# Performance work log

Measured on AMD Instinct MI355X. Metric: run time of the kernel, lower is better.

Reference implementation:

```python
import jax, jax.numpy as jnp
import numpy as np

RES = 300          # grid resolution per axis
NC_D = 16          # density_n_comp
NC_A = 48          # app_n_comp
APP_DIM = 27       # app_dim
N = 500000         # number of ray samples

MAT_MODE = [[0, 1], [0, 2], [1, 2]]
VEC_MODE = [2, 1, 0]


def setup_inputs() -> dict:
    key = jax.random.key(0)
    k0, k1, k2, k3 = jax.random.split(key, 4)
    xyz_sampled = jax.random.uniform(k0, (N, 3), minval=-1.0, maxval=1.0, dtype=jnp.float32)
    plane_coef = 0.1 * jax.random.normal(k1, (3, NC_A + NC_D, RES, RES), dtype=jnp.float32)
    line_coef = 0.1 * jax.random.normal(k2, (3, NC_A + NC_D, RES, 1), dtype=jnp.float32)
    basis_W = jax.random.normal(k3, (APP_DIM, 3 * NC_A), dtype=jnp.float32) / np.sqrt(3 * NC_A)
    return {"xyz_sampled": xyz_sampled, "plane_coef": plane_coef,
            "line_coef": line_coef, "basis_W": basis_W}


def _grid_sample(img, x, y):
    """Bilinear grid_sample, align_corners=True, zeros padding.
    img: (C, H, W); x, y: (N,) normalized coords in [-1, 1] (x -> W, y -> H).
    Returns (C, N)."""
    C, H, W = img.shape
    ix = (x + 1.0) * 0.5 * (W - 1)
    iy = (y + 1.0) * 0.5 * (H - 1)
    x0f = jnp.floor(ix)
    y0f = jnp.floor(iy)
    wx = ix - x0f   # weight for x0+1
    wy = iy - y0f   # weight for y0+1
    x0 = x0f.astype(jnp.int32)
    y0 = y0f.astype(jnp.int32)
    out = jnp.zeros((C, x.shape[0]), img.dtype)
    for dx, wxc in ((0, 1.0 - wx), (1, wx)):
        for dy, wyc in ((0, 1.0 - wy), (1, wy)):
            xi = x0 + dx
            yi = y0 + dy
            valid = (xi >= 0) & (xi < W) & (yi >= 0) & (yi < H)
            xic = jnp.clip(xi, 0, W - 1)
            yic = jnp.clip(yi, 0, H - 1)
            w = jnp.where(valid, wxc * wyc, 0.0)
            out = out + img[:, yic, xic] * w
    return out


def reference(xyz_sampled, plane_coef, line_coef, basis_W):
    zeros = jnp.zeros((xyz_sampled.shape[0],), xyz_sampled.dtype)
    pf, lf = [], []
    for i in range(3):
        m0, m1 = MAT_MODE[i]
        # plane: grid = (x=xyz[m0] -> W, y=xyz[m1] -> H)
        pf.append(_grid_sample(plane_coef[i], xyz_sampled[:, m0], xyz_sampled[:, m1]))
        # line: grid = (x=0 -> W(=1), y=xyz[vecMode] -> H) => 1D interp along H
        lf.append(_grid_sample(line_coef[i], zeros, xyz_sampled[:, VEC_MODE[i]]))
    pf = jnp.stack(pf)  # (3, NC_A+NC_D, N)
    lf = jnp.stack(lf)  # (3, NC_A+NC_D, N)
    # compute_densityfeature: last density_n_comp channels, multiply and sum-reduce
    sigma_feature = jnp.sum(pf[:, NC_A:] * lf[:, NC_A:], axis=(0, 1))  # (N,)
    # compute_appfeature: first app_n_comp channels, multiply then basis projection
    app_feats = (pf[:, :NC_A] * lf[:, :NC_A]).reshape(3 * NC_A, -1)    # (3*NC_A, N)
    app_features = app_feats.T @ basis_W.T                              # (N, APP_DIM)
    return sigma_feature, app_features
```

## Files before the change

### kernel.cpp

```cpp
#include <hip/hip_runtime.h>
#include <hip/hip_bf16.h>

#define RES 300
#define NPLANE (RES * RES)
#define NC_A 48
#define APP_DIM 27
#define KDIM 144
#define KS 168

#define NPBLK 4219

__device__ __forceinline__ float bf_lo(unsigned int u) { return __uint_as_float(u << 16); }
__device__ __forceinline__ float bf_hi(unsigned int u) { return __uint_as_float(u & 0xffff0000u); }

__global__ __launch_bounds__(256) void prep(
    const float* __restrict__ plane, const float* __restrict__ line,
    const float* __restrict__ W,
    uint2* __restrict__ TpV, unsigned int* __restrict__ TlP,
    __hip_bfloat16* __restrict__ Wg) {
  __shared__ unsigned int ltile[64 * 65];
  const int blk = blockIdx.x;
  const int tid = threadIdx.x;

  if (blk < NPBLK) {
    int flat = blk * 256 + tid;
    if (flat < 1080000) {
      int c4   = flat & 15;
      int rest = flat >> 4;
      int i  = (rest >= 45000) ? 2 : (rest >= 22500 ? 1 : 0);
      int p0 = (rest - i * 22500) * 4;
      const float* src = plane + (size_t)(i * 64 + c4 * 4) * NPLANE + p0;
      float4 r0 = *(const float4*)(src);
      float4 r1 = *(const float4*)(src + NPLANE);
      float4 r2 = *(const float4*)(src + 2 * NPLANE);
      float4 r3 = *(const float4*)(src + 3 * NPLANE);
      const float* rr[4] = {&r0.x, &r1.x, &r2.x, &r3.x};
      #pragma unroll
      for (int k = 0; k < 4; ++k) {
        __hip_bfloat162 h0, h1;
        h0.x = __float2bfloat16(rr[0][k]);
        h0.y = __float2bfloat16(rr[1][k]);
        h1.x = __float2bfloat16(rr[2][k]);
        h1.y = __float2bfloat16(rr[3][k]);
        uint2 u;
        u.x = *(unsigned int*)&h0;
        u.y = *(unsigned int*)&h1;
        TpV[((size_t)i * NPLANE + p0 + k) * 16 + c4] = u;
      }
    }
  } else if (blk < NPBLK + 15) {
    const int b  = blk - NPBLK;
    const int i  = b / 5;
    const int y0 = (b % 5) * 64;
    const int yl = tid & 63;
    const int cq = tid >> 6;
    #pragma unroll
    for (int k = 0; k < 16; ++k) {
      int c = cq * 16 + k;
      int y = y0 + yl;
      float a = 0.f, bv = 0.f;
      if (y < RES) {
        const float* row = line + (i * 64 + c) * RES;
        a  = row[y];
        bv = row[min(y + 1, RES - 1)];
      }
      __hip_bfloat162 h;
      h.x = __float2bfloat16(a);
      h.y = __float2bfloat16(bv);
      ltile[yl * 65 + c] = *(unsigned int*)&h;
    }
    __syncthreads();
    #pragma unroll
    for (int k = 0; k < 16; ++k) {
      int ylc = k * 4 + cq;
      int c   = tid & 63;
      int y   = y0 + ylc;
      if (y < RES) TlP[((size_t)i * RES + y) * 64 + c] = ltile[ylc * 65 + c];
    }
  } else {
    for (int idx = tid; idx < 2 * 5 * 64 * 8; idx += 256) {
      int j    = idx & 7;
      int lane = (idx >> 3) & 63;
      int kt   = (idx >> 9) % 5;
      int tile = idx / (5 * 64 * 8);
      int n = tile * 16 + (lane & 15);
      int k = kt * 32 + (lane >> 4) * 8 + j;
      float v = (n < APP_DIM && k < KDIM) ? W[n * KDIM + k] : 0.f;
      Wg[idx] = __float2bfloat16(v);
    }
  }
}

typedef __attribute__((ext_vector_type(8))) short short8;
typedef __attribute__((ext_vector_type(4))) float f32x4;

__global__ __launch_bounds__(256, 6) void tensorf_main(
    const float* __restrict__ xyz, const unsigned int* __restrict__ TpU,
    const unsigned int* __restrict__ TlP, const __hip_bfloat16* __restrict__ Wg,
    float* __restrict__ out, int n_total) {
  __shared__ __hip_bfloat16 prod[64 * KS];
  __shared__ float cw[64 * 18];

  const int tid  = threadIdx.x;
  const int lane = tid & 63;
  const int wave = tid >> 6;
  const int n0   = blockIdx.x * 64;

  for (int j = tid; j < 64 * 12; j += 256) {
    int s = j / 12, kk = (j % 12) * 2;
    *(unsigned int*)&prod[s * KS + KDIM + kk] = 0u;
  }

  if (tid < 64) {
    int n = min(n0 + tid, n_total - 1);
    float crd[3] = {xyz[3 * n], xyz[3 * n + 1], xyz[3 * n + 2]};
    const int m0s[3] = {0, 0, 1}, m1s[3] = {1, 2, 2}, vms[3] = {2, 1, 0};
    float* c = &cw[tid * 18];
    #pragma unroll
    for (int i = 0; i < 3; ++i) {
      float ix = fminf(fmaxf((crd[m0s[i]] + 1.f) * 149.5f, 0.f), 299.f);
      float iy = fminf(fmaxf((crd[m1s[i]] + 1.f) * 149.5f, 0.f), 299.f);
      float ly = fminf(fmaxf((crd[vms[i]] + 1.f) * 149.5f, 0.f), 299.f);
      float x0f = fminf(floorf(ix), 298.f);
      float y0f = fminf(floorf(iy), 298.f);
      float l0f = fminf(floorf(ly), 298.f);
      float wx = ix - x0f, wy = iy - y0f, lwy = ly - l0f;
      int cell = i * NPLANE + (int)y0f * RES + (int)x0f;
      int lidx = i * RES + (int)l0f;
      c[i * 6 + 0] = __int_as_float(cell | (lidx << 19));
      c[i * 6 + 1] = (1.f - wx) * (1.f - wy);
      c[i * 6 + 2] = wx * (1.f - wy);
      c[i * 6 + 3] = (1.f - wx) * wy;
      c[i * 6 + 4] = wx * wy;
      c[i * 6 + 5] = lwy;
    }
  }
  __syncthreads();

  const int cl   = lane & 31;
  const int half = lane >> 5;
  const int c2   = cl * 2;
  #pragma unroll 2
  for (int it = 0; it < 8; ++it) {
    int s = wave * 16 + it * 2 + half;
    const float* cp = &cw[s * 18];

    unsigned int u00[3], u01[3], u10[3], u11[3];
    uint2 ul[3];
    float wgt[3][5];
    #pragma unroll
    for (int i = 0; i < 3; ++i) {
      float2 q0 = *(const float2*)&cp[i * 6];
      float2 q1 = *(const float2*)&cp[i * 6 + 2];
      float2 q2 = *(const float2*)&cp[i * 6 + 4];
      int pk   = __float_as_int(q0.x);
      int cell = pk & 0x7FFFF;
      int lidx = pk >> 19;
      int bidx = cell * 32 + cl;
      u00[i] = TpU[bidx];
      u01[i] = TpU[bidx + 32];
      u10[i] = TpU[bidx + RES * 32];
      u11[i] = TpU[bidx + RES * 32 + 32];
      ul[i]  = *(const uint2*)&TlP[(lidx << 6) + c2];
      wgt[i][0] = q0.y; wgt[i][1] = q1.x; wgt[i][2] = q1.y;
      wgt[i][3] = q2.x; wgt[i][4] = q2.y;
    }

    float dsum = 0.f;
    #pragma unroll
    for (int i = 0; i < 3; ++i) {
      float pf_l = wgt[i][0] * bf_lo(u00[i]) + wgt[i][1] * bf_lo(u01[i]) +
                   wgt[i][2] * bf_lo(u10[i]) + wgt[i][3] * bf_lo(u11[i]);
      float pf_h = wgt[i][0] * bf_hi(u00[i]) + wgt[i][1] * bf_hi(u01[i]) +
                   wgt[i][2] * bf_hi(u10[i]) + wgt[i][3] * bf_hi(u11[i]);
      float lal = bf_lo(ul[i].x), lbl = bf_hi(ul[i].x);
      float lah = bf_lo(ul[i].y), lbh = bf_hi(ul[i].y);
      float lf_l = lal + wgt[i][4] * (lbl - lal);
      float lf_h = lah + wgt[i][4] * (lbh - lah);
      float prl = pf_l * lf_l, prh = pf_h * lf_h;
      if (cl < 24) {
        __hip_bfloat162 h;
        h.x = __float2bfloat16(prl);
        h.y = __float2bfloat16(prh);
        *(unsigned int*)&prod[s * KS + i * NC_A + c2] = *(unsigned int*)&h;
      } else {
        dsum += prl + prh;
      }
    }
    dsum += __shfl_xor(dsum, 1);
    dsum += __shfl_xor(dsum, 2);
    dsum += __shfl_xor(dsum, 4);
    int n = n0 + s;
    if (cl == 24 && n < n_total) out[n] = dsum;
  }
  __syncthreads();

  const int srow = lane & 15, quad = lane >> 4;
  f32x4 acc0 = {0.f, 0.f, 0.f, 0.f}, acc1 = {0.f, 0.f, 0.f, 0.f};
  const short* prodS = (const short*)prod;
  const short* WgS   = (const short*)Wg;
  const int arow = (wave * 16 + srow) * KS;
  #pragma unroll
  for (int kt = 0; kt < 5; ++kt) {
    short8 a  = *(const short8*)&prodS[arow + kt * 32 + quad * 8];
    short8 b0 = *(const short8*)&WgS[(kt * 64 + lane) * 8];
    short8 b1 = *(const short8*)&WgS[((5 + kt) * 64 + lane) * 8];
    acc0 = __builtin_amdgcn_mfma_f32_16x16x32_bf16(a, b0, acc0, 0, 0, 0);
    acc1 = __builtin_amdgcn_mfma_f32_16x16x32_bf16(a, b1, acc1, 0, 0, 0);
  }
  float* outApp = out + n_total;
  #pragma unroll
  for (int r = 0; r < 4; ++r) {
    int n = n0 + wave * 16 + quad * 4 + r;
    if (n < n_total) {
      outApp[(size_t)n * APP_DIM + srow] = acc0[r];
      if (srow < APP_DIM - 16)
        outApp[(size_t)n * APP_DIM + 16 + srow] = acc1[r];
    }
  }
}

extern "C" void kernel_launch(void* const* d_in, const int* in_sizes, int n_in,
                              void* d_out, int out_size, void* d_ws, size_t ws_size,
                              hipStream_t stream) {
  const float* xyz   = (const float*)d_in[0];
  const float* plane = (const float*)d_in[1];
  const float* line  = (const float*)d_in[2];
  const float* W     = (const float*)d_in[3];
  float* out = (float*)d_out;
  const int N = in_sizes[0] / 3;

  char* ws = (char*)d_ws;
  __hip_bfloat16* Tp  = (__hip_bfloat16*)ws;
  unsigned int*   TlP = (unsigned int*)(ws + 34560000);
  __hip_bfloat16* Wg  = (__hip_bfloat16*)(ws + 34560000 + 230400);

  prep<<<NPBLK + 16, 256, 0, stream>>>(plane, line, W, (uint2*)Tp, TlP, Wg);
  tensorf_main<<<(N + 63) / 64, 256, 0, stream>>>(
      xyz, (const unsigned int*)Tp, TlP, Wg, out, N);
}
```

Before: 227.8 us.

## Transpose plane coefficients to channel-last bf16 via LDS tiles in prep kernel

The plane-transposition stage of the prep kernel now has each block handle a 256-pixel tile of one plane for all 64 channels. It reads rows with coalesced float4 loads, converts them to bf16 and stages them in shared memory, then writes 16-byte channel-last chunks to global memory. This replaces the earlier per-thread 4-channel gather that wrote scattered 8-byte stores. The goal is fully coalesced global stores, in exchange for added LDS traffic, a barrier and possible bank conflicts on the 2-byte shared reads.

Result: no change. 228.1 us (+0.1%).

```diff
diff --git a/kernel.cpp b/kernel.cpp
--- a/kernel.cpp
+++ b/kernel.cpp
@@ -8,7 +8,9 @@
 #define KDIM 144
 #define KS 168
 
-#define NPBLK 4219
+#define PT_TILES 352
+#define NPBLK (3 * PT_TILES)
+#define LSS 268
 
 __device__ __forceinline__ float bf_lo(unsigned int u) { return __uint_as_float(u << 16); }
 __device__ __forceinline__ float bf_hi(unsigned int u) { return __uint_as_float(u & 0xffff0000u); }
@@ -16,39 +18,55 @@
 __global__ __launch_bounds__(256) void prep(
     const float* __restrict__ plane, const float* __restrict__ line,
     const float* __restrict__ W,
-    uint2* __restrict__ TpV, unsigned int* __restrict__ TlP,
+    __hip_bfloat16* __restrict__ Tp, unsigned int* __restrict__ TlP,
     __hip_bfloat16* __restrict__ Wg) {
-  __shared__ unsigned int ltile[64 * 65];
+  __shared__ unsigned short ls[64 * LSS];
   const int blk = blockIdx.x;
   const int tid = threadIdx.x;
 
   if (blk < NPBLK) {
-    int flat = blk * 256 + tid;
-    if (flat < 1080000) {
-      int c4   = flat & 15;
-      int rest = flat >> 4;
-      int i  = (rest >= 45000) ? 2 : (rest >= 22500 ? 1 : 0);
-      int p0 = (rest - i * 22500) * 4;
-      const float* src = plane + (size_t)(i * 64 + c4 * 4) * NPLANE + p0;
-      float4 r0 = *(const float4*)(src);
-      float4 r1 = *(const float4*)(src + NPLANE);
-      float4 r2 = *(const float4*)(src + 2 * NPLANE);
-      float4 r3 = *(const float4*)(src + 3 * NPLANE);
-      const float* rr[4] = {&r0.x, &r1.x, &r2.x, &r3.x};
-      #pragma unroll
-      for (int k = 0; k < 4; ++k) {
-        __hip_bfloat162 h0, h1;
-        h0.x = __float2bfloat16(rr[0][k]);
-        h0.y = __float2bfloat16(rr[1][k]);
-        h1.x = __float2bfloat16(rr[2][k]);
-        h1.y = __float2bfloat16(rr[3][k]);
-        uint2 u;
-        u.x = *(unsigned int*)&h0;
-        u.y = *(unsigned int*)&h1;
-        TpV[((size_t)i * NPLANE + p0 + k) * 16 + c4] = u;
+    const int i    = blk / PT_TILES;
+    const int p0   = (blk % PT_TILES) * 256;
+    const int l    = tid & 63;
+    const int w    = tid >> 6;
+    const int pl   = p0 + 4 * l;
+    const bool pok = (pl + 3) < NPLANE;
+    #pragma unroll
+    for (int r = 0; r < 16; ++r) {
+      int c = w * 16 + r;
+      float4 v = make_float4(0.f, 0.f, 0.f, 0.f);
+      if (pok) v = *(const float4*)&plane[(size_t)(i * 64 + c) * NPLANE + pl];
+      __hip_bfloat162 h0, h1;
+      h0.x = __float2bfloat16(v.x); h0.y = __float2bfloat16(v.y);
+      h1.x = __float2bfloat16(v.z); h1.y = __float2bfloat16(v.w);
+      uint2 u;
+      u.x = *(unsigned int*)&h0;
+      u.y = *(unsigned int*)&h1;
+      *(uint2*)&ls[c * LSS + 4 * l] = u;
+    }
+    __syncthreads();
+    const size_t obase = ((size_t)i * NPLANE + p0) * 64;
+    const int plim = min(256, NPLANE - p0);
+    #pragma unroll
+    for (int r = 0; r < 8; ++r) {
+      int flat4 = r * 256 + tid;
+      int p  = flat4 >> 3;
+      int c0 = (flat4 & 7) * 8;
+      if (p < plim) {
+        unsigned int x0 = (unsigned int)ls[(c0 + 0) * LSS + p] |
+                          ((unsigned int)ls[(c0 + 1) * LSS + p] << 16);
+        unsigned int x1 = (unsigned int)ls[(c0 + 2) * LSS + p] |
+                          ((unsigned int)ls[(c0 + 3) * LSS + p] << 16);
+        unsigned int x2 = (unsigned int)ls[(c0 + 4) * LSS + p] |
+                          ((unsigned int)ls[(c0 + 5) * LSS + p] << 16);
+        unsigned int x3 = (unsigned int)ls[(c0 + 6) * LSS + p] |
+                          ((unsigned int)ls[(c0 + 7) * LSS + p] << 16);
+        uint4 o = {x0, x1, x2, x3};
+        *(uint4*)&Tp[obase + (size_t)p * 64 + c0] = o;
       }
     }
   } else if (blk < NPBLK + 15) {
+    unsigned int* ltile = (unsigned int*)ls;
     const int b  = blk - NPBLK;
     const int i  = b / 5;
     const int y0 = (b % 5) * 64;
@@ -235,7 +253,7 @@
   unsigned int*   TlP = (unsigned int*)(ws + 34560000);
   __hip_bfloat16* Wg  = (__hip_bfloat16*)(ws + 34560000 + 230400);
 
-  prep<<<NPBLK + 16, 256, 0, stream>>>(plane, line, W, (uint2*)Tp, TlP, Wg);
+  prep<<<NPBLK + 16, 256, 0, stream>>>(plane, line, W, Tp, TlP, Wg);
   tensorf_main<<<(N + 63) / 64, 256, 0, stream>>>(
       xyz, (const unsigned int*)Tp, TlP, Wg, out, N);
 }
```
